# Kernel tuning notes

Measured on AMD Instinct MI355X. Metric: run time of the kernel, lower is better.

The kernel has to match this reference:

```python
import jax, jax.numpy as jnp
import numpy as np

B, L, D, H = 2, 2048, 1024, 16
DH = D // H
NEG = -10000.0

def setup_inputs() -> dict:
    key = jax.random.key(0)
    ks = jax.random.split(key, 6)
    scale = 1.0 / np.sqrt(D)
    inp = {
        "x": jax.random.normal(ks[0], (B, L, D), dtype=jnp.float32),
        "m": jnp.ones((B, L), dtype=jnp.int32),  # 1 = valid token, 0 = padded
        "Wq": jax.random.normal(ks[1], (D, D), dtype=jnp.float32) * scale,
        "bq": jnp.zeros((D,), dtype=jnp.float32),
        "Wk": jax.random.normal(ks[2], (D, D), dtype=jnp.float32) * scale,
        "bk": jnp.zeros((D,), dtype=jnp.float32),
        "Wv": jax.random.normal(ks[3], (D, D), dtype=jnp.float32) * scale,
        "bv": jnp.zeros((D,), dtype=jnp.float32),
        "Wp": jax.random.normal(ks[4], (D, D), dtype=jnp.float32) * scale,
        "bp": jnp.zeros((D,), dtype=jnp.float32),
    }
    return inp

def reference(x, m, Wq, bq, Wk, bk, Wv, bv, Wp, bp):
    # torch Linear: x @ W.T + b
    def heads(t):  # (B,L,D) -> (B,H,L,DH)
        return t.reshape(B, L, H, DH).transpose(0, 2, 1, 3)
    q = heads(x @ Wq.T + bq)
    k = heads(x @ Wk.T + bk)
    v = heads(x @ Wv.T + bv)
    att = jnp.einsum("bhqd,bhkd->bhqk", q, k) * (1.0 / np.sqrt(DH))  # (B,H,L,L)
    causal = jnp.tril(jnp.ones((L, L), dtype=bool))[None, None]       # (1,1,L,L)
    att = jnp.where(causal, att, NEG)
    # additive key-padding mask: 0 for valid, -10000 for padded keys
    pad = (1.0 - m.astype(att.dtype))[:, None, None, :] * NEG         # (B,1,1,L)
    att = att + pad
    att = jax.nn.softmax(att, axis=-1)
    y = jnp.einsum("bhqk,bhkd->bhqd", att, v)                          # (B,H,L,DH)
    y = y.transpose(0, 2, 1, 3).reshape(B, L, D)
    return y @ Wp.T + bp
```

## Files before the change

kernel.cpp:

```cpp
#include <hip/hip_runtime.h>
#include <hip/hip_bf16.h>

#define NB 2
#define NL 2048
#define ND 1024
#define NH 16
#define NDH 64
#define NM (NB*NL)

typedef unsigned short u16;
typedef __attribute__((ext_vector_type(8))) short short8;
typedef __attribute__((ext_vector_type(4))) float floatx4;

#define QSCALE 0.180336880f

__device__ __forceinline__ float bf2f(u16 u) {
  union { unsigned int ui; float f; } w;
  w.ui = ((unsigned int)u) << 16;
  return w.f;
}

__device__ __forceinline__ u16 f2bf(float f) {
  union { float f; unsigned int u; } v; v.f = f;
  unsigned int r = v.u + 0x7FFF + ((v.u >> 16) & 1);
  return (u16)(r >> 16);
}

__device__ __forceinline__ void async_cp16(const u16* lds, const u16* g) {
  __builtin_amdgcn_global_load_lds(
      (const __attribute__((address_space(1))) void*)g,
      (__attribute__((address_space(3))) void*)lds, 16, 0, 0);
}

__device__ __forceinline__ float dpp_xor1_f(float v) {
  return __int_as_float(__builtin_amdgcn_mov_dpp(__float_as_int(v), 0xB1, 0xF, 0xF, true));
}

__device__ __forceinline__ unsigned pk_bf16(float lo, float hi) {
  __hip_bfloat162 h2 = __float22bfloat162_rn(make_float2(lo, hi));
  return *(unsigned*)&h2;
}

#define E(qt,lo,hi,p) ((unsigned)(qt) | ((unsigned)(lo)<<8) | ((unsigned)(hi)<<16) | ((unsigned)(p)<<24))
__device__ __constant__ unsigned ATAB[64] = {
  E(20,0,10,0), E(21,0,10,0), E(21,11,21,1), E(18,0,9,0),
  E(16,0,8,0),  E(14,0,7,0),  E(10,6,10,1),  E(0,0,0,3),
  E(30,0,10,0), E(31,0,10,0), E(31,11,21,1), E(19,0,9,0),
  E(17,0,8,0),  E(15,0,7,0),  E(3,0,3,3),    E(1,0,1,3),
  E(19,10,19,1), E(20,11,20,1), E(9,0,9,3),   E(17,9,17,1),
  E(18,10,18,1), E(16,9,16,1),  E(13,0,6,0),  E(2,0,2,3),
  E(27,0,9,0),  E(28,0,9,0),  E(28,10,19,1), E(8,0,8,3),
  E(15,8,15,1), E(22,0,7,0),  E(11,0,5,0),   E(4,0,4,3),
  E(29,0,9,0),  E(29,10,19,1), E(24,0,8,0),  E(25,0,8,0),
  E(22,8,15,1), E(23,0,7,0),   E(11,6,11,1), E(12,7,12,1),
  E(29,20,29,2), E(30,11,20,1), E(25,9,17,1), E(26,0,8,0),
  E(23,8,15,1),  E(23,16,23,2), E(10,0,5,0),  E(5,0,5,3),
  E(30,21,30,2), E(31,22,31,2), E(26,9,17,1), E(26,18,26,2),
  E(13,7,13,1),  E(14,8,14,1),  E(6,0,6,3),   E(22,16,22,2),
  E(27,10,18,1), E(27,19,27,2), E(28,20,28,2), E(24,9,16,1),
  E(24,17,24,2), E(25,18,25,2), E(7,0,7,3),    E(12,0,6,0),
};

__global__ __launch_bounds__(256)
void cvt_all(const float* __restrict__ wq, const float* __restrict__ wk,
             const float* __restrict__ wv, const float* __restrict__ wp,
             const float* __restrict__ x,
             u16* __restrict__ ow, u16* __restrict__ ox)
{
  const int per4 = ND * ND / 4;
  const int tot  = 4 * per4 + NM * ND / 4;
  for (int t = blockIdx.x * 256 + threadIdx.x; t < tot; t += gridDim.x * 256) {
    const float* src; uint2* dst; int off;
    if (t < 4 * per4) {
      int w = t >> 18; off = t & (per4 - 1);
      src = (w == 0) ? wq : (w == 1) ? wk : (w == 2) ? wv : wp;
      dst = (uint2*)(ow + (size_t)w * ND * ND);
    } else {
      off = t - 4 * per4; src = x; dst = (uint2*)ox;
    }
    float4 f = ((const float4*)src)[off];
    u16 h[4] = { f2bf(f.x), f2bf(f.y), f2bf(f.z), f2bf(f.w) };
    dst[off] = *(const uint2*)h;
  }
}

#define BM 128
#define BN 128
#define BK 32
#define LDT 32

__global__ __launch_bounds__(256)
void gemm_qkv(const u16* __restrict__ A, const u16* __restrict__ Wb,
              const float* __restrict__ bq, const float* __restrict__ bk,
              const float* __restrict__ bv,
              u16* __restrict__ Qb, u16* __restrict__ Kb, u16* __restrict__ Vb)
{
  const int n0g = blockIdx.x * BN;
  const int z   = n0g >> 10;
  const int n0  = n0g & 1023;
  const u16* W    = Wb + (size_t)z * ND * ND;
  const float* Bi = (z == 0) ? bq : (z == 1) ? bk : bv;
  u16* C          = (z == 0) ? Qb : (z == 1) ? Kb : Vb;
  const float sc  = (z == 0) ? QSCALE : 1.0f;

  const int m0 = blockIdx.y * BM;
  const int tid  = threadIdx.x;
  const int lane = tid & 63;
  const int wave = tid >> 6;
  const int wm = (wave >> 1) * 64;
  const int wn = (wave & 1) * 64;
  const int quad = lane >> 4;
  const int l16  = lane & 15;

  __shared__ u16 As[BM * LDT];
  __shared__ u16 Bs[BN * LDT];

  floatx4 acc[4][4];
#pragma unroll
  for (int i = 0; i < 4; ++i)
#pragma unroll
    for (int j = 0; j < 4; ++j)
      acc[i][j] = (floatx4){0.f, 0.f, 0.f, 0.f};

  for (int k0 = 0; k0 < ND; k0 += BK) {
#pragma unroll
    for (int it = 0; it < 2; ++it) {
      int idx = tid + it * 256;
      int rr  = idx >> 2;
      int c8  = (idx & 3) << 3;
      async_cp16(&Bs[idx * 8], &W[(size_t)(n0 + rr) * ND + k0 + c8]);
      async_cp16(&As[idx * 8], &A[(size_t)(m0 + rr) * ND + k0 + c8]);
    }
    __syncthreads();

    short8 af[4], bfr[4];
#pragma unroll
    for (int i = 0; i < 4; ++i)
      af[i] = *(const short8*)&As[(wm + i * 16 + l16) * LDT + quad * 8];
#pragma unroll
    for (int j = 0; j < 4; ++j)
      bfr[j] = *(const short8*)&Bs[(wn + j * 16 + l16) * LDT + quad * 8];

#pragma unroll
    for (int i = 0; i < 4; ++i)
#pragma unroll
      for (int j = 0; j < 4; ++j)
        acc[i][j] = __builtin_amdgcn_mfma_f32_16x16x32_bf16(af[i], bfr[j], acc[i][j], 0, 0, 0);
    __syncthreads();
  }

#pragma unroll
  for (int j = 0; j < 4; ++j) {
    const int ncol = n0 + wn + j * 16 + l16;
    const float bv2 = Bi[ncol];
#pragma unroll
    for (int i = 0; i < 4; ++i) {
      const int mbase = m0 + wm + i * 16 + quad * 4;
#pragma unroll
      for (int r2 = 0; r2 < 4; ++r2) {
        float v = (acc[i][j][r2] + bv2) * sc;
        C[(size_t)(mbase + r2) * ND + ncol] = f2bf(v);
      }
    }
  }
}

#define BN2 64

__global__ __launch_bounds__(256)
void gemm_proj(const u16* __restrict__ A, const u16* __restrict__ W,
               const float* __restrict__ Bi, float* __restrict__ C)
{
  const int n0 = blockIdx.x * BN2;
  const int m0 = blockIdx.y * BM;
  const int tid  = threadIdx.x;
  const int lane = tid & 63;
  const int wave = tid >> 6;
  const int wm = (wave >> 1) * 64;
  const int wn = (wave & 1) * 32;
  const int quad = lane >> 4;
  const int l16  = lane & 15;

  __shared__ u16 As[BM * LDT];
  __shared__ u16 Bs[BN2 * LDT];

  floatx4 acc[4][2];
#pragma unroll
  for (int i = 0; i < 4; ++i)
#pragma unroll
    for (int j = 0; j < 2; ++j)
      acc[i][j] = (floatx4){0.f, 0.f, 0.f, 0.f};

  for (int k0 = 0; k0 < ND; k0 += BK) {
#pragma unroll
    for (int it = 0; it < 2; ++it) {
      int idx = tid + it * 256;
      int rr  = idx >> 2;
      int c8  = (idx & 3) << 3;
      async_cp16(&As[idx * 8], &A[(size_t)(m0 + rr) * ND + k0 + c8]);
    }
    {
      int rr = tid >> 2, c8 = (tid & 3) << 3;
      async_cp16(&Bs[tid * 8], &W[(size_t)(n0 + rr) * ND + k0 + c8]);
    }
    __syncthreads();

    short8 af[4], bfr[2];
#pragma unroll
    for (int i = 0; i < 4; ++i)
      af[i] = *(const short8*)&As[(wm + i * 16 + l16) * LDT + quad * 8];
#pragma unroll
    for (int j = 0; j < 2; ++j)
      bfr[j] = *(const short8*)&Bs[(wn + j * 16 + l16) * LDT + quad * 8];

#pragma unroll
    for (int i = 0; i < 4; ++i)
#pragma unroll
      for (int j = 0; j < 2; ++j)
        acc[i][j] = __builtin_amdgcn_mfma_f32_16x16x32_bf16(af[i], bfr[j], acc[i][j], 0, 0, 0);
    __syncthreads();
  }

#pragma unroll
  for (int j = 0; j < 2; ++j) {
    const int ncol = n0 + wn + j * 16 + l16;
    const float bv2 = Bi[ncol];
#pragma unroll
    for (int i = 0; i < 4; ++i) {
      const int mbase = m0 + wm + i * 16 + quad * 4;
#pragma unroll
      for (int r2 = 0; r2 < 4; ++r2)
        C[(size_t)(mbase + r2) * ND + ncol] = acc[i][j][r2] + bv2;
    }
  }
}

#define TSTR 66
__global__ __launch_bounds__(256)
void vtrans(const u16* __restrict__ V, u16* __restrict__ VT)
{
  const int lt = blockIdx.x;
  const int bh = blockIdx.y;
  const int b = bh >> 4, h = bh & 15;
  const int l0 = lt * 64;
  const int tid = threadIdx.x;
  __shared__ u16 Ls[64][TSTR];
#pragma unroll
  for (int p = 0; p < 2; ++p) {
    int idx = tid + p * 256;
    int r = idx >> 3, c = (idx & 7) << 3;
    *(uint4*)&Ls[r][c] = *(const uint4*)&V[(size_t)(b * NL + l0 + r) * ND + h * NDH + c];
  }
  __syncthreads();
#pragma unroll
  for (int p = 0; p < 2; ++p) {
    int idx = tid + p * 256;
    int lg = idx & 7, d = idx >> 3;
    u16 tb[8];
#pragma unroll
    for (int e = 0; e < 8; ++e) tb[e] = Ls[lg * 8 + e][d];
    *(uint4*)&VT[((size_t)(b * NH + h) * NDH + d) * NL + l0 + lg * 8] = *(const uint4*)tb;
  }
}

#define KC 64
#define PSTR 72

__global__ __launch_bounds__(256)
void attn_mfma(const u16* __restrict__ Q, const u16* __restrict__ K,
               const u16* __restrict__ VT, const int* __restrict__ msk,
               u16* __restrict__ Y, u16* __restrict__ PO0, u16* __restrict__ PO1,
               float* __restrict__ PL)
{
  const int t = blockIdx.x;
  const int r = t >> 8;
  const int s = t & 255;
  const int xcd = s & 7;
  const int v = s >> 3;
  const int bh = xcd * 4 + (v & 3);
  const int g = v >> 2;

  const unsigned e = ATAB[(g << 3) | r];
  const int qt   = e & 255;
  const int lo   = (e >> 8) & 255;
  const int hi   = (e >> 16) & 255;
  const int part = e >> 24;

  const int b = bh >> 4;
  const int h = bh & 15;
  const int q0 = qt * 64;
  const int tid  = threadIdx.x;
  const int lane = tid & 63;
  const int wave = tid >> 6;
  const int wq   = wave * 16;
  const int quad = lane >> 4;
  const int l16  = lane & 15;

  __shared__ u16 KP[64 * PSTR];
  __shared__ u16 Vt[NDH * 64];

  const u16* Kbase  = K  + (size_t)b * NL * ND + h * NDH;
  const u16* VTbase = VT + (size_t)(b * NH + h) * NDH * NL;
  const int* mbase  = msk + b * NL;

  short8 qf[2];
#pragma unroll
  for (int kk = 0; kk < 2; ++kk)
    qf[kk] = *(const short8*)&Q[(size_t)(b * NL + q0 + wq + l16) * ND
                                + h * NDH + kk * 32 + quad * 8];

  short8 onesf;
  {
    const short ov = (l16 == 0) ? (short)0x3F80 : (short)0;
#pragma unroll
    for (int ee = 0; ee < 8; ++ee) onesf[ee] = ov;
  }

  floatx4 o[4];
#pragma unroll
  for (int ot = 0; ot < 4; ++ot) o[ot] = (floatx4){0.f, 0.f, 0.f, 0.f};
  floatx4 lacc = (floatx4){0.f, 0.f, 0.f, 0.f};

  const int odd = l16 & 1;
  const int sw  = l16 & 7;
  const int rowb = q0 + wq + quad * 4;

  auto chunk_body = [&](int k0, bool diag) {
#pragma unroll
    for (int pp = 0; pp < 2; ++pp) {
      int sl = tid + pp * 256;
      int rr = sl >> 3;
      int ch = (sl & 7) ^ (rr & 7);
      async_cp16(&KP[sl * 8], Kbase + (size_t)(k0 + rr) * ND + ch * 8);
      async_cp16(&Vt[sl * 8], VTbase + (size_t)rr * NL + k0 + ch * 8);
    }
    __syncthreads();

    int mm[4];
#pragma unroll
    for (int ct = 0; ct < 4; ++ct) mm[ct] = mbase[k0 + ct * 16 + l16];

    floatx4 sc4[4];
#pragma unroll
    for (int ct = 0; ct < 4; ++ct) {
      const u16* krow = &KP[(ct * 16 + l16) * 64];
      short8 kf0 = *(const short8*)(krow + ((quad ^ sw) << 3));
      short8 kf1 = *(const short8*)(krow + (((4 | quad) ^ sw) << 3));
      floatx4 a = (floatx4){0.f, 0.f, 0.f, 0.f};
      a = __builtin_amdgcn_mfma_f32_16x16x32_bf16(qf[0], kf0, a, 0, 0, 0);
      a = __builtin_amdgcn_mfma_f32_16x16x32_bf16(qf[1], kf1, a, 0, 0, 0);
      sc4[ct] = a;
    }
    __syncthreads();

#pragma unroll
    for (int ct = 0; ct < 4; ++ct) {
      const float pmul = (float)mm[ct];
      float pv[4];
#pragma unroll
      for (int r2 = 0; r2 < 4; ++r2) {
        float pr = pmul * __builtin_amdgcn_exp2f(sc4[ct][r2]);
        if (diag) {
          const int col = k0 + ct * 16 + l16;
          pr = (col > rowb + r2) ? 0.f : pr;
        }
        pv[r2] = pr;
      }
      float nb0 = dpp_xor1_f(pv[0]), nb1 = dpp_xor1_f(pv[1]);
      float nb2 = dpp_xor1_f(pv[2]), nb3 = dpp_xor1_f(pv[3]);
      const int colb  = ct * 16 + (l16 & ~1);
      const int row01 = wq + quad * 4 + odd;
      unsigned d01 = odd ? pk_bf16(nb1, pv[1]) : pk_bf16(pv[0], nb0);
      unsigned d23 = odd ? pk_bf16(nb3, pv[3]) : pk_bf16(pv[2], nb2);
      *(unsigned*)&KP[row01 * PSTR + colb]       = d01;
      *(unsigned*)&KP[(row01 + 2) * PSTR + colb] = d23;
    }

#pragma unroll
    for (int kk = 0; kk < 2; ++kk) {
      short8 pf = *(const short8*)&KP[(wq + l16) * PSTR + kk * 32 + quad * 8];
#pragma unroll
      for (int ot = 0; ot < 4; ++ot) {
        const u16* vrow = &Vt[(ot * 16 + l16) * 64];
        short8 vf = *(const short8*)(vrow + ((((kk << 2) | quad) ^ sw) << 3));
        o[ot] = __builtin_amdgcn_mfma_f32_16x16x32_bf16(pf, vf, o[ot], 0, 0, 0);
      }
      lacc = __builtin_amdgcn_mfma_f32_16x16x32_bf16(pf, onesf, lacc, 0, 0, 0);
    }
    __syncthreads();
  };

  for (int kc = lo; kc < hi; ++kc) chunk_body(kc * KC, false);
  chunk_body(hi * KC, hi == qt);

  if (part == 3) {
    float inv[4];
#pragma unroll
    for (int r2 = 0; r2 < 4; ++r2) {
      const float l = __shfl(lacc[r2], quad << 4);
      inv[r2] = 1.0f / l;
    }
#pragma unroll
    for (int ot = 0; ot < 4; ++ot)
#pragma unroll
      for (int r2 = 0; r2 < 4; ++r2) {
        const int row = q0 + wq + quad * 4 + r2;
        Y[(size_t)(b * NL + row) * ND + h * NDH + ot * 16 + l16] = f2bf(o[ot][r2] * inv[r2]);
      }
  } else {
    const int base = (qt < 22) ? (qt - 10) * 2 : 24 + (qt - 22) * 3;
    const int slot = bh * 54 + base + part;
    u16* po = (slot < 1024) ? PO0 + (size_t)slot * 4096
                            : PO1 + (size_t)(slot - 1024) * 4096;
#pragma unroll
    for (int ot = 0; ot < 4; ++ot)
#pragma unroll
      for (int r2 = 0; r2 < 4; ++r2)
        po[(wq + quad * 4 + r2) * 64 + ot * 16 + l16] = f2bf(o[ot][r2]);
    if (l16 == 0) {
#pragma unroll
      for (int r2 = 0; r2 < 4; ++r2)
        PL[slot * 64 + wq + quad * 4 + r2] = lacc[r2];
    }
  }
}

__global__ __launch_bounds__(256)
void attn_combine(const u16* __restrict__ PO0, const u16* __restrict__ PO1,
                  const float* __restrict__ PL, u16* __restrict__ Y)
{
  const int tt = blockIdx.x;
  const int bh = tt / 22;
  const int qt = 10 + (tt - bh * 22);
  const int b = bh >> 4, h = bh & 15;
  const int tid = threadIdx.x;
  const int row = tid >> 2, cg = (tid & 3) << 4;
  const int nparts = (qt < 22) ? 2 : 3;
  const int base = bh * 54 + ((qt < 22) ? (qt - 10) * 2 : 24 + (qt - 22) * 3);

  float acc[16];
#pragma unroll
  for (int e = 0; e < 16; ++e) acc[e] = 0.f;
  float l = 0.f;

  for (int p = 0; p < nparts; ++p) {
    const int slot = base + p;
    const u16* po = (slot < 1024) ? PO0 + (size_t)slot * 4096
                                  : PO1 + (size_t)(slot - 1024) * 4096;
    const u16* src = po + row * 64 + cg;
    uint4 a0 = *(const uint4*)src, a1 = *(const uint4*)(src + 8);
    const u16* ap = (const u16*)&a0;
#pragma unroll
    for (int e = 0; e < 8; ++e) acc[e] += bf2f(ap[e]);
    ap = (const u16*)&a1;
#pragma unroll
    for (int e = 0; e < 8; ++e) acc[8 + e] += bf2f(ap[e]);
    l += PL[slot * 64 + row];
  }

  const float inv = 1.0f / l;
  u16 outv[16];
#pragma unroll
  for (int e = 0; e < 16; ++e) outv[e] = f2bf(acc[e] * inv);
  u16* y = Y + (size_t)(b * NL + qt * 64 + row) * ND + h * NDH + cg;
  *(uint4*)y = *(const uint4*)outv;
  *(uint4*)(y + 8) = *(const uint4*)(outv + 8);
}

extern "C" void kernel_launch(void* const* d_in, const int* in_sizes, int n_in,
                              void* d_out, int out_size, void* d_ws, size_t ws_size,
                              hipStream_t stream) {
  const float* x  = (const float*)d_in[0];
  const int*   m  = (const int*)d_in[1];
  const float* Wq = (const float*)d_in[2];
  const float* bq = (const float*)d_in[3];
  const float* Wk = (const float*)d_in[4];
  const float* bk = (const float*)d_in[5];
  const float* Wv = (const float*)d_in[6];
  const float* bv = (const float*)d_in[7];
  const float* Wp = (const float*)d_in[8];
  const float* bp = (const float*)d_in[9];
  float* out = (float*)d_out;

  const size_t per = (size_t)NM * ND;
  u16* Qb = (u16*)d_ws;
  u16* Kb = Qb + per;
  u16* Vb = Kb + per;
  u16* Wb = Vb + per;
  u16* Yb = Qb;
  u16* xb = (u16*)d_out;
  u16* VTb = xb + per;
  u16* PO0 = xb;
  u16* PO1 = Vb;
  float* PL = (float*)(Vb + 3 * 1024 * 1024);

  cvt_all<<<2048, 256, 0, stream>>>(Wq, Wk, Wv, Wp, x, Wb, xb);

  gemm_qkv<<<dim3(3 * ND / BN, NM / BM), 256, 0, stream>>>(
      xb, Wb, bq, bk, bv, Qb, Kb, Vb);

  vtrans<<<dim3(NL / 64, NB * NH), 256, 0, stream>>>(Vb, VTb);

  attn_mfma<<<2048, 256, 0, stream>>>(Qb, Kb, VTb, m, Yb, PO0, PO1, PL);

  attn_combine<<<704, 256, 0, stream>>>(PO0, PO1, PL, Yb);

  const u16* Wpb = Wb + 3 * (size_t)ND * ND;
  gemm_proj<<<dim3(ND / BN2, NM / BM), 256, 0, stream>>>(Yb, Wpb, bp, out);
}
```

Before: 195.5 us.

## Double attention query tile to 128 rows and rebuild split-K work table

Each attention block now handles 128 query rows instead of 64, with every wave covering two 16-row sub-blocks. Each K/V chunk staged in LDS therefore feeds twice as many MFMAs, which cuts global loads and barriers per unit of work. The causal load-balancing table is rebuilt for 16 query tiles, split into up to 4 parts, and padded with no-op entries that make those blocks return early. The combine kernel and the partial-output buffers are resized to match, and part of the buffer now lives in the bf16 weight workspace that is no longer needed. In exchange, register and LDS use per block go up and the grid shrinks, which may lower occupancy.

```diff
diff --git a/kernel.cpp b/kernel.cpp
--- a/kernel.cpp
+++ b/kernel.cpp
@@ -42,24 +42,21 @@
 }
 
 #define E(qt,lo,hi,p) ((unsigned)(qt) | ((unsigned)(lo)<<8) | ((unsigned)(hi)<<16) | ((unsigned)(p)<<24))
-__device__ __constant__ unsigned ATAB[64] = {
-  E(20,0,10,0), E(21,0,10,0), E(21,11,21,1), E(18,0,9,0),
-  E(16,0,8,0),  E(14,0,7,0),  E(10,6,10,1),  E(0,0,0,3),
-  E(30,0,10,0), E(31,0,10,0), E(31,11,21,1), E(19,0,9,0),
-  E(17,0,8,0),  E(15,0,7,0),  E(3,0,3,3),    E(1,0,1,3),
-  E(19,10,19,1), E(20,11,20,1), E(9,0,9,3),   E(17,9,17,1),
-  E(18,10,18,1), E(16,9,16,1),  E(13,0,6,0),  E(2,0,2,3),
-  E(27,0,9,0),  E(28,0,9,0),  E(28,10,19,1), E(8,0,8,3),
-  E(15,8,15,1), E(22,0,7,0),  E(11,0,5,0),   E(4,0,4,3),
-  E(29,0,9,0),  E(29,10,19,1), E(24,0,8,0),  E(25,0,8,0),
-  E(22,8,15,1), E(23,0,7,0),   E(11,6,11,1), E(12,7,12,1),
-  E(29,20,29,2), E(30,11,20,1), E(25,9,17,1), E(26,0,8,0),
-  E(23,8,15,1),  E(23,16,23,2), E(10,0,5,0),  E(5,0,5,3),
-  E(30,21,30,2), E(31,22,31,2), E(26,9,17,1), E(26,18,26,2),
-  E(13,7,13,1),  E(14,8,14,1),  E(6,0,6,3),   E(22,16,22,2),
-  E(27,10,18,1), E(27,19,27,2), E(28,20,28,2), E(24,9,16,1),
-  E(24,17,24,2), E(25,18,25,2), E(7,0,7,3),    E(12,0,6,0),
+#define XX 0xFFFFFFFFu
+__device__ __constant__ unsigned ATAB[40] = {
+  E(15,0,8,0),   E(15,9,17,1),  E(8,0,8,0),    E(13,0,6,0),   XX,
+  E(12,0,8,0),   E(12,9,17,1),  E(12,18,25,2), E(11,0,7,0),   XX,
+  E(8,9,17,1),   E(13,7,13,1),  E(13,14,20,2), E(13,21,27,3), E(1,0,3,7),
+  E(14,0,7,0),   E(14,8,15,1),  E(11,8,15,1),  E(3,0,7,7),    E(0,0,1,7),
+  E(11,16,23,2), E(7,0,7,0),    E(15,18,24,2), E(5,0,5,0),    E(4,0,4,0),
+  E(10,0,7,0),   E(7,8,15,1),   E(15,25,31,3), E(5,6,11,1),   E(4,5,9,1),
+  E(14,16,22,2), E(14,23,29,3), E(10,8,14,1),  E(9,0,6,0),    E(2,0,5,7),
+  E(10,15,21,2), E(9,7,13,1),   E(6,0,6,0),    E(6,7,13,1),   E(9,14,19,2),
 };
+__device__ __constant__ unsigned char PBASE[16] =
+  {0,0,0,0, 0,2,4,6,8, 10,13,16,19, 22,26,30};
+__device__ __constant__ unsigned char NPARTS[16] =
+  {0,0,0,0, 2,2,2,2,2, 3,3,3,3, 4,4,4};
 
 __global__ __launch_bounds__(256)
 void cvt_all(const float* __restrict__ wq, const float* __restrict__ wk,
@@ -270,17 +267,15 @@
 void attn_mfma(const u16* __restrict__ Q, const u16* __restrict__ K,
                const u16* __restrict__ VT, const int* __restrict__ msk,
                u16* __restrict__ Y, u16* __restrict__ PO0, u16* __restrict__ PO1,
-               float* __restrict__ PL)
+               u16* __restrict__ PO2, float* __restrict__ PL)
 {
-  const int t = blockIdx.x;
-  const int r = t >> 8;
-  const int s = t & 255;
+  const unsigned e = ATAB[(((blockIdx.x & 255) >> 3 >> 2) * 5) + (blockIdx.x >> 8)];
+  if (e == XX) return;
+  const int s = blockIdx.x & 255;
   const int xcd = s & 7;
   const int v = s >> 3;
   const int bh = xcd * 4 + (v & 3);
-  const int g = v >> 2;
-
-  const unsigned e = ATAB[(g << 3) | r];
+
   const int qt   = e & 255;
   const int lo   = (e >> 8) & 255;
   const int hi   = (e >> 16) & 255;
@@ -288,26 +283,28 @@
 
   const int b = bh >> 4;
   const int h = bh & 15;
-  const int q0 = qt * 64;
+  const int q0 = qt * 128;
   const int tid  = threadIdx.x;
   const int lane = tid & 63;
   const int wave = tid >> 6;
-  const int wq   = wave * 16;
+  const int wq   = wave * 32;
   const int quad = lane >> 4;
   const int l16  = lane & 15;
 
-  __shared__ u16 KP[64 * PSTR];
+  __shared__ u16 KP[128 * PSTR];
   __shared__ u16 Vt[NDH * 64];
 
   const u16* Kbase  = K  + (size_t)b * NL * ND + h * NDH;
   const u16* VTbase = VT + (size_t)(b * NH + h) * NDH * NL;
   const int* mbase  = msk + b * NL;
 
-  short8 qf[2];
-#pragma unroll
-  for (int kk = 0; kk < 2; ++kk)
-    qf[kk] = *(const short8*)&Q[(size_t)(b * NL + q0 + wq + l16) * ND
-                                + h * NDH + kk * 32 + quad * 8];
+  short8 qf[2][2];
+#pragma unroll
+  for (int rb = 0; rb < 2; ++rb)
+#pragma unroll
+    for (int kk = 0; kk < 2; ++kk)
+      qf[rb][kk] = *(const short8*)&Q[(size_t)(b * NL + q0 + wq + rb * 16 + l16) * ND
+                                      + h * NDH + kk * 32 + quad * 8];
 
   short8 onesf;
   {
@@ -316,14 +313,17 @@
     for (int ee = 0; ee < 8; ++ee) onesf[ee] = ov;
   }
 
-  floatx4 o[4];
-#pragma unroll
-  for (int ot = 0; ot < 4; ++ot) o[ot] = (floatx4){0.f, 0.f, 0.f, 0.f};
-  floatx4 lacc = (floatx4){0.f, 0.f, 0.f, 0.f};
+  floatx4 o[2][4];
+#pragma unroll
+  for (int rb = 0; rb < 2; ++rb)
+#pragma unroll
+    for (int ot = 0; ot < 4; ++ot) o[rb][ot] = (floatx4){0.f, 0.f, 0.f, 0.f};
+  floatx4 lacc[2];
+  lacc[0] = (floatx4){0.f, 0.f, 0.f, 0.f};
+  lacc[1] = (floatx4){0.f, 0.f, 0.f, 0.f};
 
   const int odd = l16 & 1;
   const int sw  = l16 & 7;
-  const int rowb = q0 + wq + quad * 4;
 
   auto chunk_body = [&](int k0, bool diag) {
 #pragma unroll
@@ -340,131 +340,156 @@
 #pragma unroll
     for (int ct = 0; ct < 4; ++ct) mm[ct] = mbase[k0 + ct * 16 + l16];
 
-    floatx4 sc4[4];
+    floatx4 sc4[2][4];
 #pragma unroll
     for (int ct = 0; ct < 4; ++ct) {
       const u16* krow = &KP[(ct * 16 + l16) * 64];
       short8 kf0 = *(const short8*)(krow + ((quad ^ sw) << 3));
       short8 kf1 = *(const short8*)(krow + (((4 | quad) ^ sw) << 3));
-      floatx4 a = (floatx4){0.f, 0.f, 0.f, 0.f};
-      a = __builtin_amdgcn_mfma_f32_16x16x32_bf16(qf[0], kf0, a, 0, 0, 0);
-      a = __builtin_amdgcn_mfma_f32_16x16x32_bf16(qf[1], kf1, a, 0, 0, 0);
-      sc4[ct] = a;
-    }
-    __syncthreads();
-
-#pragma unroll
-    for (int ct = 0; ct < 4; ++ct) {
-      const float pmul = (float)mm[ct];
-      float pv[4];
-#pragma unroll
-      for (int r2 = 0; r2 < 4; ++r2) {
-        float pr = pmul * __builtin_amdgcn_exp2f(sc4[ct][r2]);
-        if (diag) {
-          const int col = k0 + ct * 16 + l16;
-          pr = (col > rowb + r2) ? 0.f : pr;
+#pragma unroll
+      for (int rb = 0; rb < 2; ++rb) {
+        floatx4 a = (floatx4){0.f, 0.f, 0.f, 0.f};
+        a = __builtin_amdgcn_mfma_f32_16x16x32_bf16(qf[rb][0], kf0, a, 0, 0, 0);
+        a = __builtin_amdgcn_mfma_f32_16x16x32_bf16(qf[rb][1], kf1, a, 0, 0, 0);
+        sc4[rb][ct] = a;
+      }
+    }
+    __syncthreads();
+
+#pragma unroll
+    for (int rb = 0; rb < 2; ++rb) {
+      const int rowb = q0 + wq + rb * 16 + quad * 4;
+#pragma unroll
+      for (int ct = 0; ct < 4; ++ct) {
+        const float pmul = (float)mm[ct];
+        float pv[4];
+#pragma unroll
+        for (int r2 = 0; r2 < 4; ++r2) {
+          float pr = pmul * __builtin_amdgcn_exp2f(sc4[rb][ct][r2]);
+          if (diag) {
+            const int col = k0 + ct * 16 + l16;
+            pr = (col > rowb + r2) ? 0.f : pr;
+          }
+          pv[r2] = pr;
         }
-        pv[r2] = pr;
+        float nb0 = dpp_xor1_f(pv[0]), nb1 = dpp_xor1_f(pv[1]);
+        float nb2 = dpp_xor1_f(pv[2]), nb3 = dpp_xor1_f(pv[3]);
+        const int colb  = ct * 16 + (l16 & ~1);
+        const int row01 = wq + rb * 16 + quad * 4 + odd;
+        unsigned d01 = odd ? pk_bf16(nb1, pv[1]) : pk_bf16(pv[0], nb0);
+        unsigned d23 = odd ? pk_bf16(nb3, pv[3]) : pk_bf16(pv[2], nb2);
+        *(unsigned*)&KP[row01 * PSTR + colb]       = d01;
+        *(unsigned*)&KP[(row01 + 2) * PSTR + colb] = d23;
       }
-      float nb0 = dpp_xor1_f(pv[0]), nb1 = dpp_xor1_f(pv[1]);
-      float nb2 = dpp_xor1_f(pv[2]), nb3 = dpp_xor1_f(pv[3]);
-      const int colb  = ct * 16 + (l16 & ~1);
-      const int row01 = wq + quad * 4 + odd;
-      unsigned d01 = odd ? pk_bf16(nb1, pv[1]) : pk_bf16(pv[0], nb0);
-      unsigned d23 = odd ? pk_bf16(nb3, pv[3]) : pk_bf16(pv[2], nb2);
-      *(unsigned*)&KP[row01 * PSTR + colb]       = d01;
-      *(unsigned*)&KP[(row01 + 2) * PSTR + colb] = d23;
     }
 
 #pragma unroll
     for (int kk = 0; kk < 2; ++kk) {
-      short8 pf = *(const short8*)&KP[(wq + l16) * PSTR + kk * 32 + quad * 8];
+      short8 pf[2];
+#pragma unroll
+      for (int rb = 0; rb < 2; ++rb)
+        pf[rb] = *(const short8*)&KP[(wq + rb * 16 + l16) * PSTR + kk * 32 + quad * 8];
 #pragma unroll
       for (int ot = 0; ot < 4; ++ot) {
         const u16* vrow = &Vt[(ot * 16 + l16) * 64];
         short8 vf = *(const short8*)(vrow + ((((kk << 2) | quad) ^ sw) << 3));
-        o[ot] = __builtin_amdgcn_mfma_f32_16x16x32_bf16(pf, vf, o[ot], 0, 0, 0);
+#pragma unroll
+        for (int rb = 0; rb < 2; ++rb)
+          o[rb][ot] = __builtin_amdgcn_mfma_f32_16x16x32_bf16(pf[rb], vf, o[rb][ot], 0, 0, 0);
       }
-      lacc = __builtin_amdgcn_mfma_f32_16x16x32_bf16(pf, onesf, lacc, 0, 0, 0);
+      lacc[0] = __builtin_amdgcn_mfma_f32_16x16x32_bf16(pf[0], onesf, lacc[0], 0, 0, 0);
+      lacc[1] = __builtin_amdgcn_mfma_f32_16x16x32_bf16(pf[1], onesf, lacc[1], 0, 0, 0);
     }
     __syncthreads();
   };
 
-  for (int kc = lo; kc < hi; ++kc) chunk_body(kc * KC, false);
-  chunk_body(hi * KC, hi == qt);
-
-  if (part == 3) {
-    float inv[4];
-#pragma unroll
-    for (int r2 = 0; r2 < 4; ++r2) {
-      const float l = __shfl(lacc[r2], quad << 4);
-      inv[r2] = 1.0f / l;
-    }
-#pragma unroll
-    for (int ot = 0; ot < 4; ++ot)
+  const int dstart = 2 * qt;
+  for (int kc = lo; kc <= hi; ++kc) chunk_body(kc * KC, kc >= dstart);
+
+  if (part == 7) {
+#pragma unroll
+    for (int rb = 0; rb < 2; ++rb) {
+      float inv[4];
 #pragma unroll
       for (int r2 = 0; r2 < 4; ++r2) {
-        const int row = q0 + wq + quad * 4 + r2;
-        Y[(size_t)(b * NL + row) * ND + h * NDH + ot * 16 + l16] = f2bf(o[ot][r2] * inv[r2]);
+        const float l = __shfl(lacc[rb][r2], quad << 4);
+        inv[r2] = 1.0f / l;
       }
+#pragma unroll
+      for (int ot = 0; ot < 4; ++ot)
+#pragma unroll
+        for (int r2 = 0; r2 < 4; ++r2) {
+          const int row = q0 + wq + rb * 16 + quad * 4 + r2;
+          Y[(size_t)(b * NL + row) * ND + h * NDH + ot * 16 + l16] =
+              f2bf(o[rb][ot][r2] * inv[r2]);
+        }
+    }
   } else {
-    const int base = (qt < 22) ? (qt - 10) * 2 : 24 + (qt - 22) * 3;
-    const int slot = bh * 54 + base + part;
-    u16* po = (slot < 1024) ? PO0 + (size_t)slot * 4096
-                            : PO1 + (size_t)(slot - 1024) * 4096;
-#pragma unroll
-    for (int ot = 0; ot < 4; ++ot)
-#pragma unroll
-      for (int r2 = 0; r2 < 4; ++r2)
-        po[(wq + quad * 4 + r2) * 64 + ot * 16 + l16] = f2bf(o[ot][r2]);
+    const int slot = bh * 34 + (int)PBASE[qt] + part;
+    u16* po = (slot < 512) ? PO0 + (size_t)slot * 8192
+            : (slot < 1024) ? PO1 + (size_t)(slot - 512) * 8192
+                            : PO2 + (size_t)(slot - 1024) * 8192;
+#pragma unroll
+    for (int rb = 0; rb < 2; ++rb)
+#pragma unroll
+      for (int ot = 0; ot < 4; ++ot)
+#pragma unroll
+        for (int r2 = 0; r2 < 4; ++r2)
+          po[(wq + rb * 16 + quad * 4 + r2) * 64 + ot * 16 + l16] = f2bf(o[rb][ot][r2]);
     if (l16 == 0) {
 #pragma unroll
-      for (int r2 = 0; r2 < 4; ++r2)
-        PL[slot * 64 + wq + quad * 4 + r2] = lacc[r2];
+      for (int rb = 0; rb < 2; ++rb)
+#pragma unroll
+        for (int r2 = 0; r2 < 4; ++r2)
+          PL[slot * 128 + wq + rb * 16 + quad * 4 + r2] = lacc[rb][r2];
     }
   }
 }
 
 __global__ __launch_bounds__(256)
 void attn_combine(const u16* __restrict__ PO0, const u16* __restrict__ PO1,
-                  const float* __restrict__ PL, u16* __restrict__ Y)
+                  const u16* __restrict__ PO2, const float* __restrict__ PL,
+                  u16* __restrict__ Y)
 {
   const int tt = blockIdx.x;
-  const int bh = tt / 22;
-  const int qt = 10 + (tt - bh * 22);
+  const int bh = tt / 12;
+  const int qt = 4 + (tt - bh * 12);
   const int b = bh >> 4, h = bh & 15;
   const int tid = threadIdx.x;
-  const int row = tid >> 2, cg = (tid & 3) << 4;
-  const int nparts = (qt < 22) ? 2 : 3;
-  const int base = bh * 54 + ((qt < 22) ? (qt - 10) * 2 : 24 + (qt - 22) * 3);
-
-  float acc[16];
-#pragma unroll
-  for (int e = 0; e < 16; ++e) acc[e] = 0.f;
-  float l = 0.f;
-
-  for (int p = 0; p < nparts; ++p) {
-    const int slot = base + p;
-    const u16* po = (slot < 1024) ? PO0 + (size_t)slot * 4096
-                                  : PO1 + (size_t)(slot - 1024) * 4096;
-    const u16* src = po + row * 64 + cg;
-    uint4 a0 = *(const uint4*)src, a1 = *(const uint4*)(src + 8);
-    const u16* ap = (const u16*)&a0;
-#pragma unroll
-    for (int e = 0; e < 8; ++e) acc[e] += bf2f(ap[e]);
-    ap = (const u16*)&a1;
-#pragma unroll
-    for (int e = 0; e < 8; ++e) acc[8 + e] += bf2f(ap[e]);
-    l += PL[slot * 64 + row];
-  }
-
-  const float inv = 1.0f / l;
-  u16 outv[16];
-#pragma unroll
-  for (int e = 0; e < 16; ++e) outv[e] = f2bf(acc[e] * inv);
-  u16* y = Y + (size_t)(b * NL + qt * 64 + row) * ND + h * NDH + cg;
-  *(uint4*)y = *(const uint4*)outv;
-  *(uint4*)(y + 8) = *(const uint4*)(outv + 8);
+  const int np = (int)NPARTS[qt];
+  const int base = bh * 34 + (int)PBASE[qt];
+
+#pragma unroll
+  for (int rp = 0; rp < 2; ++rp) {
+    const int row = rp * 64 + (tid >> 2);
+    const int cg  = (tid & 3) << 4;
+    float acc[16];
+#pragma unroll
+    for (int e2 = 0; e2 < 16; ++e2) acc[e2] = 0.f;
+    float l = 0.f;
+    for (int p = 0; p < np; ++p) {
+      const int slot = base + p;
+      const u16* po = (slot < 512) ? PO0 + (size_t)slot * 8192
+                    : (slot < 1024) ? PO1 + (size_t)(slot - 512) * 8192
+                                    : PO2 + (size_t)(slot - 1024) * 8192;
+      const u16* src = po + row * 64 + cg;
+      uint4 a0 = *(const uint4*)src, a1 = *(const uint4*)(src + 8);
+      const u16* ap = (const u16*)&a0;
+#pragma unroll
+      for (int e2 = 0; e2 < 8; ++e2) acc[e2] += bf2f(ap[e2]);
+      ap = (const u16*)&a1;
+#pragma unroll
+      for (int e2 = 0; e2 < 8; ++e2) acc[8 + e2] += bf2f(ap[e2]);
+      l += PL[slot * 128 + row];
+    }
+    const float inv = 1.0f / l;
+    u16 outv[16];
+#pragma unroll
+    for (int e2 = 0; e2 < 16; ++e2) outv[e2] = f2bf(acc[e2] * inv);
+    u16* y = Y + (size_t)(b * NL + qt * 128 + row) * ND + h * NDH + cg;
+    *(uint4*)y = *(const uint4*)outv;
+    *(uint4*)(y + 8) = *(const uint4*)(outv + 8);
+  }
 }
 
 extern "C" void kernel_launch(void* const* d_in, const int* in_sizes, int n_in,
@@ -492,7 +517,8 @@
   u16* VTb = xb + per;
   u16* PO0 = xb;
   u16* PO1 = Vb;
-  float* PL = (float*)(Vb + 3 * 1024 * 1024);
+  u16* PO2 = Wb;
+  float* PL = (float*)(Wb + 512 * 1024);
 
   cvt_all<<<2048, 256, 0, stream>>>(Wq, Wk, Wv, Wp, x, Wb, xb);
 
@@ -501,9 +527,9 @@
 
   vtrans<<<dim3(NL / 64, NB * NH), 256, 0, stream>>>(Vb, VTb);
 
-  attn_mfma<<<2048, 256, 0, stream>>>(Qb, Kb, VTb, m, Yb, PO0, PO1, PL);
-
-  attn_combine<<<704, 256, 0, stream>>>(PO0, PO1, PL, Yb);
+  attn_mfma<<<1280, 256, 0, stream>>>(Qb, Kb, VTb, m, Yb, PO0, PO1, PO2, PL);
+
+  attn_combine<<<384, 256, 0, stream>>>(PO0, PO1, PO2, PL, Yb);
 
   const u16* Wpb = Wb + 3 * (size_t)ND * ND;
   gemm_proj<<<dim3(ND / BN2, NM / BM), 256, 0, stream>>>(Yb, Wpb, bp, out);
```

Measured after the change: 200.5 us. +2.6%, slower.
